# Performance work log

Measured on AMD Instinct MI355X. Metric: run time of the kernel, lower is better.

The kernel has to match this reference:

```python
import jax, jax.numpy as jnp
import numpy as np

B = 524288      # batch
D = 16          # ds_dim
N = 32          # number of dynamical systems
H = 128         # gating hidden width


def setup_inputs() -> dict:
    key = jax.random.key(0)
    ks = jax.random.split(key, 8)
    x_cur = jax.random.normal(ks[0], (B, D), dtype=jnp.float32)
    W1 = jax.random.normal(ks[1], (H, D), dtype=jnp.float32) * 0.1
    b1 = jax.random.normal(ks[2], (H,), dtype=jnp.float32) * 0.1
    W2 = jax.random.normal(ks[3], (N, H), dtype=jnp.float32) * 0.1
    b2 = jax.random.normal(ks[4], (N,), dtype=jnp.float32) * 0.1
    # B matrices are PSD (geotorch.positive_semidefinite), C are skew-symmetric (geotorch.skew)
    Braw = jax.random.normal(ks[5], (N, D, D), dtype=jnp.float32) * 0.3
    B_mats = jnp.einsum('nij,nkj->nik', Braw, Braw)  # PSD: R R^T
    Craw = jax.random.normal(ks[6], (N, D, D), dtype=jnp.float32) * 0.3
    C_mats = 0.5 * (Craw - jnp.swapaxes(Craw, -1, -2))  # skew-symmetric
    x_target = jax.random.normal(ks[7], (1, D), dtype=jnp.float32)
    return {"x_cur": x_cur, "W1": W1, "b1": b1, "W2": W2, "b2": b2,
            "B_mats": B_mats, "C_mats": C_mats, "x_target": x_target}


def reference(x_cur, W1, b1, W2, b2, B_mats, C_mats, x_target):
    # gating weights: softmax(Linear -> ReLU -> Linear)
    h = jax.nn.relu(x_cur @ W1.T + b1)          # [B, H]
    w_all = jax.nn.softmax(h @ W2.T + b2, axis=1)  # [B, N]
    # per-system linear map A_i = B_i + C_i applied to (x* - x)
    A = B_mats + C_mats                          # [N, D, D]
    diff = x_target - x_cur                      # [B, D]
    # torch.mm(A, diff.T).T == diff @ A.T -> proj[b,n,k] = sum_d A[n,k,d] diff[b,d]
    proj = jnp.einsum('nkd,bd->bnk', A, diff)    # [B, N, D]
    out = jnp.einsum('bn,bnk->bk', w_all, proj)  # [B, D]
    return out
```

## Files before the change

kernel.cpp:

```cpp
#include <hip/hip_runtime.h>

#define BATCH 524288

typedef __bf16 bf16x8 __attribute__((ext_vector_type(8)));
typedef float f32x4 __attribute__((ext_vector_type(4)));
typedef float f32x8 __attribute__((ext_vector_type(8)));

#define SMEM_BYTES (16640 + 4 * 8704)

__device__ __forceinline__ f32x8 load8(const float* __restrict__ p) {
    float4 a = *(const float4*)p;
    float4 b = *(const float4*)(p + 4);
    f32x8 v = {a.x, a.y, a.z, a.w, b.x, b.y, b.z, b.w};
    return v;
}

__global__ __launch_bounds__(256, 3) void andp_v3(
    const float* __restrict__ x_cur,
    const float* __restrict__ W1,
    const float* __restrict__ b1,
    const float* __restrict__ W2,
    const float* __restrict__ b2,
    const float* __restrict__ Bm,
    const float* __restrict__ Cm,
    const float* __restrict__ x_t,
    float* __restrict__ out)
{
    extern __shared__ char smem[];
    __bf16* sA2 = (__bf16*)smem;
    const int tid = threadIdx.x;

#pragma unroll
    for (int i = 0; i < 32; ++i) {
        int idx = tid + i * 256;
        int n = idx >> 8, k = (idx >> 4) & 15, d = idx & 15;
        sA2[k * 520 + n * 16 + d] = (__bf16)(Bm[idx] + Cm[idx]);
    }

    const int wave = tid >> 6, lane = tid & 63;
    const int c = lane & 15, q = lane >> 4;
    const int qh = q >> 1;
    const int hh = (q & 1) * 8;

    __bf16* hsw = (__bf16*)(smem + 16640 + wave * 8704);
    float*  wsw = (float*)hsw;

    bf16x8 w1f[8];
#pragma unroll
    for (int t = 0; t < 8; ++t) {
        f32x8 v = {0.f,0.f,0.f,0.f,0.f,0.f,0.f,0.f};
        if (q < 2) v = load8(W1 + (t * 16 + c) * 16 + q * 8);
        w1f[t] = __builtin_convertvector(v, bf16x8);
    }
    bf16x8 w2f[2][4];
#pragma unroll
    for (int t2 = 0; t2 < 2; ++t2)
#pragma unroll
        for (int kk = 0; kk < 4; ++kk)
            w2f[t2][kk] = __builtin_convertvector(
                load8(W2 + (t2 * 16 + c) * 128 + kk * 32 + q * 8), bf16x8);

    float b1v[8];
#pragma unroll
    for (int t = 0; t < 8; ++t) b1v[t] = b1[t * 16 + c];
    float b2v[2][4];
#pragma unroll
    for (int t2 = 0; t2 < 2; ++t2)
#pragma unroll
        for (int r = 0; r < 4; ++r) b2v[t2][r] = b2[t2 * 16 + q * 4 + r];
    const f32x8 xtv = load8(x_t + hh);

    __syncthreads();

    const int blk_row = blockIdx.x * 256 + wave * 64;
    const f32x4 z4 = {0.f, 0.f, 0.f, 0.f};

    for (int p = 0; p < 2; ++p) {
        const int r0 = blk_row + p * 32;

        bf16x8 af[2];
        f32x8 dif[2];
#pragma unroll
        for (int t01 = 0; t01 < 2; ++t01) {
            f32x8 xv = load8(x_cur + (size_t)(r0 + t01 * 16 + c) * 16 + hh);
            af[t01]  = __builtin_convertvector(xv, bf16x8);
            dif[t01] = xtv - xv;
        }

#pragma unroll
        for (int t01 = 0; t01 < 2; ++t01) {
            f32x4 acc1[8];
#pragma unroll
            for (int t = 0; t < 8; ++t)
                acc1[t] = __builtin_amdgcn_mfma_f32_16x16x32_bf16(af[t01], w1f[t], z4, 0, 0, 0);
#pragma unroll
            for (int t = 0; t < 8; ++t)
#pragma unroll
                for (int r = 0; r < 4; ++r) {
                    float v = fmaxf(acc1[t][r] + b1v[t], 0.f);
                    hsw[(t01 * 16 + q * 4 + r) * 136 + t * 16 + c] = (__bf16)v;
                }

            f32x4 acc2[2];
            acc2[0] = z4; acc2[1] = z4;
#pragma unroll
            for (int kk = 0; kk < 4; ++kk) {
                bf16x8 hb = *(const bf16x8*)(hsw + (t01 * 16 + c) * 136 + kk * 32 + q * 8);
                acc2[0] = __builtin_amdgcn_mfma_f32_16x16x32_bf16(w2f[0][kk], hb, acc2[0], 0, 0, 0);
                acc2[1] = __builtin_amdgcn_mfma_f32_16x16x32_bf16(w2f[1][kk], hb, acc2[1], 0, 0, 0);
            }

            float l[8];
#pragma unroll
            for (int t2 = 0; t2 < 2; ++t2)
#pragma unroll
                for (int r = 0; r < 4; ++r) l[t2 * 4 + r] = acc2[t2][r] + b2v[t2][r];
            float mx = l[0];
#pragma unroll
            for (int i = 1; i < 8; ++i) mx = fmaxf(mx, l[i]);
            mx = fmaxf(mx, __shfl_xor(mx, 16, 64));
            mx = fmaxf(mx, __shfl_xor(mx, 32, 64));
            float e[8], s = 0.f;
#pragma unroll
            for (int i = 0; i < 8; ++i) { e[i] = __expf(l[i] - mx); s += e[i]; }
            s += __shfl_xor(s, 16, 64);
            s += __shfl_xor(s, 32, 64);
            float inv = 1.0f / s;
#pragma unroll
            for (int t2 = 0; t2 < 2; ++t2)
#pragma unroll
                for (int r = 0; r < 4; ++r)
                    wsw[(t01 * 16 + c) * 33 + t2 * 16 + q * 4 + r] = e[t2 * 4 + r] * inv;
        }

        f32x4 acc3[2];
        acc3[0] = z4; acc3[1] = z4;
#pragma unroll
        for (int kk = 0; kk < 16; ++kk) {
            float w0 = wsw[c * 33 + 2 * kk + qh];
            float w1 = wsw[(16 + c) * 33 + 2 * kk + qh];
            bf16x8 bfr = *(const bf16x8*)(sA2 + c * 520 + kk * 32 + q * 8);
            bf16x8 a0 = __builtin_convertvector(dif[0] * w0, bf16x8);
            bf16x8 a1 = __builtin_convertvector(dif[1] * w1, bf16x8);
            acc3[0] = __builtin_amdgcn_mfma_f32_16x16x32_bf16(a0, bfr, acc3[0], 0, 0, 0);
            acc3[1] = __builtin_amdgcn_mfma_f32_16x16x32_bf16(a1, bfr, acc3[1], 0, 0, 0);
        }

#pragma unroll
        for (int t01 = 0; t01 < 2; ++t01) {
            float* op = out + (size_t)(r0 + t01 * 16 + q * 4) * 16 + c;
#pragma unroll
            for (int r = 0; r < 4; ++r) op[r * 16] = acc3[t01][r];
        }
    }
}

extern "C" void kernel_launch(void* const* d_in, const int* in_sizes, int n_in,
                              void* d_out, int out_size, void* d_ws, size_t ws_size,
                              hipStream_t stream) {
    const float* x_cur = (const float*)d_in[0];
    const float* W1    = (const float*)d_in[1];
    const float* b1    = (const float*)d_in[2];
    const float* W2    = (const float*)d_in[3];
    const float* b2    = (const float*)d_in[4];
    const float* Bm    = (const float*)d_in[5];
    const float* Cm    = (const float*)d_in[6];
    const float* x_t   = (const float*)d_in[7];
    float* out = (float*)d_out;

    const int blocks = BATCH / 256;
    andp_v3<<<blocks, 256, SMEM_BYTES, stream>>>(
        x_cur, W1, b1, W2, b2, Bm, Cm, x_t, out);
}
```

Measured before the change: 134.3 us.

## Pass softmax weights via ds_bpermute, halve per-wave LDS, raise occupancy

```diff
diff --git a/kernel.cpp b/kernel.cpp
--- a/kernel.cpp
+++ b/kernel.cpp
@@ -3,10 +3,12 @@
 #define BATCH 524288
 
 typedef __bf16 bf16x8 __attribute__((ext_vector_type(8)));
+typedef __bf16 bf16x2 __attribute__((ext_vector_type(2)));
 typedef float f32x4 __attribute__((ext_vector_type(4)));
 typedef float f32x8 __attribute__((ext_vector_type(8)));
+typedef float f32x2 __attribute__((ext_vector_type(2)));
 
-#define SMEM_BYTES (16640 + 4 * 8704)
+#define SMEM_BYTES (16640 + 4 * 4352)
 
 __device__ __forceinline__ f32x8 load8(const float* __restrict__ p) {
     float4 a = *(const float4*)p;
@@ -15,7 +17,13 @@
     return v;
 }
 
-__global__ __launch_bounds__(256, 3) void andp_v3(
+__device__ __forceinline__ int pack2bf(float a, float b) {
+    f32x2 v = {a, b};
+    bf16x2 p = __builtin_convertvector(v, bf16x2);
+    return __builtin_bit_cast(int, p);
+}
+
+__global__ __launch_bounds__(256, 4) void andp_v4(
     const float* __restrict__ x_cur,
     const float* __restrict__ W1,
     const float* __restrict__ b1,
@@ -41,9 +49,12 @@
     const int c = lane & 15, q = lane >> 4;
     const int qh = q >> 1;
     const int hh = (q & 1) * 8;
+    const int tflip = qh & 1;
+    const int qx2 = q ^ (2 * ((c >> 3) & 1));
+    const int c4 = c * 4;
+    const int sh = qh ? 0 : 16;
 
-    __bf16* hsw = (__bf16*)(smem + 16640 + wave * 8704);
-    float*  wsw = (float*)hsw;
+    __bf16* hsw = (__bf16*)(smem + 16640 + wave * 4352);
 
     bf16x8 w1f[8];
 #pragma unroll
@@ -75,6 +86,7 @@
     const int blk_row = blockIdx.x * 256 + wave * 64;
     const f32x4 z4 = {0.f, 0.f, 0.f, 0.f};
 
+#pragma unroll
     for (int p = 0; p < 2; ++p) {
         const int r0 = blk_row + p * 32;
 
@@ -87,6 +99,8 @@
             dif[t01] = xtv - xv;
         }
 
+        int wpk[2][4];
+
 #pragma unroll
         for (int t01 = 0; t01 < 2; ++t01) {
             f32x4 acc1[8];
@@ -94,18 +108,20 @@
             for (int t = 0; t < 8; ++t)
                 acc1[t] = __builtin_amdgcn_mfma_f32_16x16x32_bf16(af[t01], w1f[t], z4, 0, 0, 0);
 #pragma unroll
-            for (int t = 0; t < 8; ++t)
+            for (int t = 0; t < 8; ++t) {
+                const int colb = (t ^ tflip) * 16 + c;
 #pragma unroll
                 for (int r = 0; r < 4; ++r) {
                     float v = fmaxf(acc1[t][r] + b1v[t], 0.f);
-                    hsw[(t01 * 16 + q * 4 + r) * 136 + t * 16 + c] = (__bf16)v;
+                    hsw[(q * 4 + r) * 136 + colb] = (__bf16)v;
                 }
+            }
 
             f32x4 acc2[2];
             acc2[0] = z4; acc2[1] = z4;
 #pragma unroll
             for (int kk = 0; kk < 4; ++kk) {
-                bf16x8 hb = *(const bf16x8*)(hsw + (t01 * 16 + c) * 136 + kk * 32 + q * 8);
+                bf16x8 hb = *(const bf16x8*)(hsw + c * 136 + kk * 32 + qx2 * 8);
                 acc2[0] = __builtin_amdgcn_mfma_f32_16x16x32_bf16(w2f[0][kk], hb, acc2[0], 0, 0, 0);
                 acc2[1] = __builtin_amdgcn_mfma_f32_16x16x32_bf16(w2f[1][kk], hb, acc2[1], 0, 0, 0);
             }
@@ -129,16 +145,21 @@
 #pragma unroll
             for (int t2 = 0; t2 < 2; ++t2)
 #pragma unroll
-                for (int r = 0; r < 4; ++r)
-                    wsw[(t01 * 16 + c) * 33 + t2 * 16 + q * 4 + r] = e[t2 * 4 + r] * inv;
+                for (int rp = 0; rp < 2; ++rp)
+                    wpk[t01][t2 * 2 + rp] =
+                        pack2bf(e[t2 * 4 + 2 * rp] * inv, e[t2 * 4 + 2 * rp + 1] * inv);
         }
 
         f32x4 acc3[2];
         acc3[0] = z4; acc3[1] = z4;
 #pragma unroll
         for (int kk = 0; kk < 16; ++kk) {
-            float w0 = wsw[c * 33 + 2 * kk + qh];
-            float w1 = wsw[(16 + c) * 33 + 2 * kk + qh];
+            const int widx = (kk >> 3) * 2 + (kk & 1);
+            const int bpi = c4 + ((kk >> 1) & 3) * 64;
+            int bp0 = __builtin_amdgcn_ds_bpermute(bpi, wpk[0][widx]);
+            int bp1 = __builtin_amdgcn_ds_bpermute(bpi, wpk[1][widx]);
+            float w0 = __builtin_bit_cast(float, (unsigned)(bp0 << sh) & 0xffff0000u);
+            float w1 = __builtin_bit_cast(float, (unsigned)(bp1 << sh) & 0xffff0000u);
             bf16x8 bfr = *(const bf16x8*)(sA2 + c * 520 + kk * 32 + q * 8);
             bf16x8 a0 = __builtin_convertvector(dif[0] * w0, bf16x8);
             bf16x8 a1 = __builtin_convertvector(dif[1] * w1, bf16x8);
@@ -169,6 +190,6 @@
     float* out = (float*)d_out;
 
     const int blocks = BATCH / 256;
-    andp_v3<<<blocks, 256, SMEM_BYTES, stream>>>(
+    andp_v4<<<blocks, 256, SMEM_BYTES, stream>>>(
         x_cur, W1, b1, W2, b2, Bm, Cm, x_t, out);
 }
```

After: 197.1 us. +46.7%, slower.
